# Kernel optimization log

Measured on AMD Instinct MI355X. Metric: run time of the kernel, lower is better.

The kernel has to match this reference:

```python
import jax, jax.numpy as jnp
import numpy as np

D = 256
H = 8
DH = D // H
TANH_CLIP = 10.0
NEG_INF = -1e9


def setup_inputs() -> dict:
    key = jax.random.key(0)
    ks = jax.random.split(key, 7)
    B, T, N = 32, 512, 512
    s = 1.0 / np.sqrt(D)
    return {
        "embeddings": jax.random.normal(ks[0], (B, N, D), dtype=jnp.float32),
        "current_nodes": jax.random.randint(ks[1], (B, T), 0, N, dtype=jnp.int64),
        "action_mask": jax.random.randint(ks[2], (B, T, N), 0, 2) > 0,
        "W_node": jax.random.normal(ks[3], (D, 3 * D), dtype=jnp.float32) * s,
        "W_fixed": jax.random.normal(ks[4], (D, D), dtype=jnp.float32) * s,
        "W_step": jax.random.normal(ks[5], (D, D), dtype=jnp.float32) * s,
        "W_out": jax.random.normal(ks[6], (D, D), dtype=jnp.float32) * s,
    }


def reference(embeddings, current_nodes, action_mask, W_node, W_fixed, W_step, W_out):
    """Batched equivalent of the autoregressive pointer-attention decode loop.

    embeddings: [B, N, D]; current_nodes: [B, T]; action_mask: [B, T, N] (True = feasible).
    Returns log_p: [B, T, N].
    """
    B, N, _ = embeddings.shape
    # ---- _precompute_cache ----
    proj = embeddings @ W_node                      # [B, N, 3D]
    glimpse_k, glimpse_v, logit_k = jnp.split(proj, 3, axis=-1)
    graph_context = jnp.mean(embeddings, axis=1) @ W_fixed   # [B, D]

    # ---- step context (gather current node embedding, project) ----
    step_emb = jnp.take_along_axis(embeddings, current_nodes[..., None], axis=1)  # [B, T, D]
    glimpse_q = step_emb @ W_step + graph_context[:, None, :]                      # [B, T, D]

    # ---- multi-head glimpse attention (one query per decode step) ----
    q = glimpse_q.reshape(B, -1, H, DH)
    k = glimpse_k.reshape(B, N, H, DH)
    v = glimpse_v.reshape(B, N, H, DH)
    scores = jnp.einsum("bthd,bnhd->bhtn", q, k) / np.sqrt(DH)
    scores = jnp.where(action_mask[:, None, :, :], scores, NEG_INF)
    attn = jax.nn.softmax(scores, axis=-1)
    heads = jnp.einsum("bhtn,bnhd->bthd", attn, v).reshape(B, -1, D)
    glimpse = heads @ W_out                                                        # [B, T, D]

    # ---- pointer logits: tanh clipping, mask, log-softmax ----
    logits = jnp.einsum("btd,bnd->btn", glimpse, logit_k) / np.sqrt(D)
    logits = TANH_CLIP * jnp.tanh(logits)
    logits = jnp.where(action_mask, logits, NEG_INF)
    return jax.nn.log_softmax(logits, axis=-1)
```

## Files before the change

kernel.cpp:

```cpp
#include <hip/hip_runtime.h>
#include <hip/hip_bf16.h>

constexpr int BB = 32;
constexpr int TT = 512;
constexpr int NN = 512;
constexpr int DD = 256;
constexpr int HH = 8;
constexpr int DH = 32;
#define NEG_INF (-1e9f)

#define QSCL 0.25505872f
#define LSCL 0.18033688f
#define MBF16 ((ushort)0xCE6E)

typedef __attribute__((ext_vector_type(8))) short bf16x8;
typedef __attribute__((ext_vector_type(4))) float f32x4;

__device__ inline float ex2(float x) { return __builtin_amdgcn_exp2f(x); }

__device__ inline ushort f2bf(float x) {
    union { float f; unsigned u; } c; c.f = x;
    unsigned u = c.u + 0x7fffu + ((c.u >> 16) & 1u);
    return (ushort)(u >> 16);
}
__device__ inline uint pk2t(float a, float b) {
    return __builtin_amdgcn_perm(__float_as_uint(b), __float_as_uint(a),
                                 0x07060302u);
}
__device__ inline ushort tr16(float x) { return (ushort)(__float_as_uint(x) >> 16); }
__device__ inline float bf2f(ushort u) {
    union { uint u; float f; } c; c.u = (uint)u << 16; return c.f;
}
__device__ inline void gload_lds16(const void* g, void* l) {
    __builtin_amdgcn_global_load_lds(
        (const __attribute__((address_space(1))) unsigned int*)g,
        (__attribute__((address_space(3))) unsigned int*)l, 16, 0, 0);
}

__global__ __launch_bounds__(256) void prep_all_k(
    const float* __restrict__ emb, ushort* __restrict__ embB,
    float* __restrict__ partial, const float* __restrict__ Wn,
    const float* __restrict__ Ws, const float* __restrict__ Wo,
    ushort* __restrict__ WnT, ushort* __restrict__ WsT,
    ushort* __restrict__ WoT, const int* __restrict__ mask,
    uint* __restrict__ mbt) {
    int j = blockIdx.x;
    int tid = threadIdx.x;
    if (j < 256) {
        int b = j >> 3, part = j & 7, d = tid;
        const float* eb = emb + ((size_t)b * NN + part * 64) * DD + d;
        ushort* ob = embB + ((size_t)b * NN + part * 64) * DD + d;
        float s = 0.f;
        #pragma unroll 4
        for (int i = 0; i < 64; i++) {
            float v = eb[(size_t)i * DD];
            s += v;
            ob[(size_t)i * DD] = f2bf(v);
        }
        partial[((size_t)b * 8 + part) * DD + d] = s;
    } else if (j < 576) {
        __shared__ float t[32][33];
        int g = j - 256;
        int gx = g % 40, gy = g / 40;
        const float* W;
        ushort* WT;
        int NC, xb;
        if (gx < 24)      { W = Wn; WT = WnT; NC = 768; xb = gx; }
        else if (gx < 32) { W = Ws; WT = WsT; NC = 256; xb = gx - 24; }
        else              { W = Wo; WT = WoT; NC = 256; xb = gx - 32; }
        int tx = tid & 31, ty = tid >> 5;
        int x = xb * 32 + tx;
        int y0 = gy * 32;
        #pragma unroll
        for (int i = 0; i < 4; i++)
            t[ty + i * 8][tx] = W[(size_t)(y0 + ty + i * 8) * NC + x];
        __syncthreads();
        #pragma unroll
        for (int i = 0; i < 4; i++)
            WT[(size_t)(xb * 32 + ty + i * 8) * 256 + y0 + tx] =
                f2bf(t[tx][ty + i * 8]);
    } else {
        int idx = (j - 576) * 256 + tid;
        int row = idx >> 4, w = idx & 15;
        const int* mr = mask + (size_t)row * NN + w;
        uint u = 0;
        #pragma unroll
        for (int c = 0; c < 32; c++) u |= (uint)(mr[c * 16] != 0) << c;
        mbt[idx] = u;
    }
}

template <int TASK>
__global__ __launch_bounds__(256) void gemm3_k(
    const ushort* __restrict__ A0, const ushort* __restrict__ WT0,
    const ushort* __restrict__ WT1, ushort* __restrict__ O0,
    ushort* __restrict__ O1, ushort* __restrict__ O2,
    ushort* __restrict__ O3, const float* __restrict__ partial,
    const float* __restrict__ Wf, const int* __restrict__ cur) {
    int j = blockIdx.x;
    bool k2 = (TASK == 0) && (j >= 1536);
    int bx, by;
    if (TASK == 0 && !k2) {
        int x = j & 7, t = j >> 3;
        bx = x * 16 + t / 12; by = t % 12;
    } else {
        int jj = k2 ? j - 1536 : j;
        int x = jj & 7, t = jj >> 3;
        bx = x * 16 + (t >> 2); by = t & 3;
    }
    int row0 = bx * 128, col0 = by * 64;
    int tid = threadIdx.x;
    int w = tid >> 6, l = tid & 63;
    int lo = l & 15, hi = l >> 4;

    __shared__ ushort As[2][128 * 64];
    __shared__ ushort Bs[2][64 * 64];
    __shared__ float ctxs[64];

    const ushort* WT = k2 ? WT1 : WT0;

    auto stage = [&](int buf, int kk) {
        #pragma unroll
        for (int i = 0; i < 4; i++) {
            int u = i * 256 + tid;
            int row = u >> 3, slot = u & 7;
            int arow = row0 + row;
            const ushort* ap;
            if (k2) {
                int b = arow >> 9;
                ap = A0 + ((size_t)(b * NN + cur[arow])) * DD;
            } else {
                ap = A0 + (size_t)arow * DD;
            }
            const void* gsrc = ap + kk * 64 + ((slot ^ (row & 7)) << 3);
            void* ldst = (char*)&As[buf][0] + i * 4096 + w * 1024;
            gload_lds16(gsrc, ldst);
        }
        #pragma unroll
        for (int i = 0; i < 2; i++) {
            int u = i * 256 + tid;
            int row = u >> 3, slot = u & 7;
            const void* gsrc =
                WT + (size_t)(col0 + row) * 256 + kk * 64 + ((slot ^ (row & 7)) << 3);
            void* ldst = (char*)&Bs[buf][0] + i * 4096 + w * 1024;
            gload_lds16(gsrc, ldst);
        }
    };

    const f32x4 zero = {0.f, 0.f, 0.f, 0.f};
    f32x4 acc[2][4] = {{zero, zero, zero, zero}, {zero, zero, zero, zero}};

    stage(0, 0);
    __syncthreads();
    #pragma unroll
    for (int kk = 0; kk < 4; kk++) {
        if (kk < 3) stage((kk + 1) & 1, kk + 1);
        int cb = kk & 1;
        #pragma unroll
        for (int ks = 0; ks < 2; ks++) {
            int sx = ((ks * 4 + hi) ^ (lo & 7)) << 4;
            bf16x8 af0 = *(const bf16x8*)((char*)&As[cb][0] + (w * 32 + lo) * 128 + sx);
            bf16x8 af1 = *(const bf16x8*)((char*)&As[cb][0] + (w * 32 + 16 + lo) * 128 + sx);
            #pragma unroll
            for (int c = 0; c < 4; c++) {
                bf16x8 bf = *(const bf16x8*)((char*)&Bs[cb][0] + (c * 16 + lo) * 128 + sx);
                acc[0][c] = __builtin_amdgcn_mfma_f32_16x16x32_bf16(af0, bf, acc[0][c], 0, 0, 0);
                acc[1][c] = __builtin_amdgcn_mfma_f32_16x16x32_bf16(af1, bf, acc[1][c], 0, 0, 0);
            }
        }
        __syncthreads();
    }

    int bbq = row0 >> 9;
    if (k2) {
        float* fs = (float*)&As[0][0];
        float mk = 0.f;
        #pragma unroll
        for (int p = 0; p < 8; p++)
            mk += partial[(size_t)bbq * 2048 + p * 256 + tid];
        fs[tid] = mk * (1.0f / 512.0f);
        __syncthreads();
        int cc = tid & 63, part = tid >> 6;
        float cs = 0.f;
        #pragma unroll 16
        for (int k = part * 64; k < part * 64 + 64; k++)
            cs += fs[k] * Wf[(size_t)k * 256 + col0 + cc];
        float* fs2 = fs + 256;
        fs2[part * 64 + cc] = cs;
        __syncthreads();
        if (tid < 64)
            ctxs[tid] = fs2[tid] + fs2[64 + tid] + fs2[128 + tid] + fs2[192 + tid];
        __syncthreads();
    }

    #pragma unroll
    for (int rg = 0; rg < 2; rg++) {
        int rw0 = row0 + w * 32 + rg * 16;
        int bb = rw0 >> 9;
        #pragma unroll
        for (int c = 0; c < 4; c++) {
            int col = col0 + c * 16 + lo;
            float v[4];
            #pragma unroll
            for (int r = 0; r < 4; r++) v[r] = acc[rg][c][r];
            if constexpr (TASK == 0) {
                if (k2) {
                    float bv = ctxs[col - col0];
                    #pragma unroll
                    for (int r = 0; r < 4; r++)
                        O3[(size_t)(rw0 + 4 * hi + r) * DD + col] =
                            f2bf((v[r] + bv) * QSCL);
                } else if (col < 256) {
                    int head = col >> 5, dh = col & 31;
                    #pragma unroll
                    for (int r = 0; r < 4; r++) {
                        int n = (rw0 + 4 * hi + r) & (NN - 1);
                        O0[(((size_t)(bb * HH + head) * NN + n) << 5) + dh] = f2bf(v[r]);
                    }
                } else if (col < 512) {
                    int cc2 = col - 256;
                    int bhv = bb * HH + (cc2 >> 5);
                    int dh = cc2 & 31;
                    int n0 = (rw0 + 4 * hi) & (NN - 1);
                    int m = n0 >> 2;
                    int p_ = m >> 3, s_ = (m >> 2) & 1, g_ = m & 3;
                    int n0p = (8 * p_ + 2 * g_ + s_) << 2;
                    ushort4 uv = {f2bf(v[0]), f2bf(v[1]), f2bf(v[2]), f2bf(v[3])};
                    *(ushort4*)(O1 + ((size_t)bhv * DH + dh) * NN + n0p) = uv;
                } else {
                    #pragma unroll
                    for (int r = 0; r < 4; r++)
                        O2[(size_t)(rw0 + 4 * hi + r) * 256 + (col - 512)] =
                            f2bf(v[r] * LSCL);
                }
            } else {
                #pragma unroll
                for (int r = 0; r < 4; r++)
                    O0[(size_t)(rw0 + 4 * hi + r) * DD + col] = f2bf(v[r]);
            }
        }
    }
}

__global__ __launch_bounds__(256, 4) void attn12_k(
    const ushort* __restrict__ gq, const ushort* __restrict__ gkT,
    const ushort* __restrict__ vTp, const uint* __restrict__ mbt,
    ushort* __restrict__ headsB) {
    int j = blockIdx.x;
    int bh = j & 255, quarter = j >> 8;
    int b = bh >> 3, h = bh & 7;
    int tid = threadIdx.x;
    int w = tid >> 6, l = tid & 63;
    int lo = l & 15, hi = l >> 4;

    __shared__ ushort Ks[8192];
    __shared__ ushort Vs[8192];
    __shared__ ushort OT[4][16][40];

    const f32x4 zero = {0.f, 0.f, 0.f, 0.f};
    const bf16x8 ones = {(short)0x3F80, (short)0x3F80, (short)0x3F80,
                         (short)0x3F80, (short)0x3F80, (short)0x3F80,
                         (short)0x3F80, (short)0x3F80};
    int q0 = quarter * 128;
    int kswz = (lo & 7) << 4;

    bf16x8 qf0 = *(const bf16x8*)(gq + ((size_t)(b * TT + q0 + w * 16 + lo)) * DD + h * DH + hi * 8);
    bf16x8 qf1 = *(const bf16x8*)(gq + ((size_t)(b * TT + q0 + 64 + w * 16 + lo)) * DD + h * DH + hi * 8);
    uint4 mq0 = *(const uint4*)(mbt + ((size_t)(b * TT + q0 + w * 16 + lo)) * 16 + 4 * hi);
    uint4 mq1 = *(const uint4*)(mbt + ((size_t)(b * TT + q0 + 64 + w * 16 + lo)) * 16 + 4 * hi);

    f32x4 o0[2] = {zero, zero};
    f32x4 o1[2] = {zero, zero};
    f32x4 osum[2] = {zero, zero};

    const char* kbase = (const char*)(gkT + (size_t)bh * (NN * DH));
    const char* vbase = (const char*)(vTp + (size_t)bh * (DH * NN));

    for (int ph = 0; ph < 2; ph++) {
        if (ph) __syncthreads();
        {
            const char* ksrc = kbase + ph * 16384;
            #pragma unroll
            for (int i = 0; i < 4; i++) {
                int x = (i * 256 + tid) * 16;
                int g = x ^ (((x >> 2) & 0x70) ^ ((x >> 4) & 0x10));
                gload_lds16(ksrc + g, (char*)Ks + i * 4096 + w * 1024);
            }
        }
        {
            const char* vsrc = vbase + ph * 512;
            #pragma unroll
            for (int i = 0; i < 4; i++) {
                int x = (i * 256 + tid) * 16;
                int g = ((x >> 9) << 10) + ((x & 511) ^ ((x >> 5) & 0x70));
                gload_lds16(vsrc + g, (char*)Vs + i * 4096 + w * 1024);
            }
        }
        __syncthreads();

        #pragma unroll
        for (int qc2 = 0; qc2 < 2; qc2++) {
            bf16x8 qf = qc2 ? qf1 : qf0;
            uint4 mq = qc2 ? mq1 : mq0;

            #pragma unroll 4
            for (int p = 0; p < 8; p++) {
                int nn = 32 * p + lo;
                bf16x8 kf0 = *(const bf16x8*)((char*)Ks + ((nn * 64 + hi * 16) ^ kswz));
                bf16x8 kf1 = *(const bf16x8*)((char*)Ks + (((nn + 16) * 64 + hi * 16) ^ kswz));
                __builtin_amdgcn_s_setprio(1);
                f32x4 s0 = __builtin_amdgcn_mfma_f32_16x16x32_bf16(kf0, qf, zero, 0, 0, 0);
                f32x4 s1 = __builtin_amdgcn_mfma_f32_16x16x32_bf16(kf1, qf, zero, 0, 0, 0);
                __builtin_amdgcn_s_setprio(0);
                union { bf16x8 v; uint u[4]; } pf;
                {
                    int c = ph * 16 + 2 * p;
                    float e0 = ((mq.x >> c) & 1u) ? ex2(s0[0]) : 0.f;
                    float e1 = ((mq.y >> c) & 1u) ? ex2(s0[1]) : 0.f;
                    float e2 = ((mq.z >> c) & 1u) ? ex2(s0[2]) : 0.f;
                    float e3 = ((mq.w >> c) & 1u) ? ex2(s0[3]) : 0.f;
                    pf.u[0] = pk2t(e0, e1);
                    pf.u[1] = pk2t(e2, e3);
                }
                {
                    int c = ph * 16 + 2 * p + 1;
                    float e0 = ((mq.x >> c) & 1u) ? ex2(s1[0]) : 0.f;
                    float e1 = ((mq.y >> c) & 1u) ? ex2(s1[1]) : 0.f;
                    float e2 = ((mq.z >> c) & 1u) ? ex2(s1[2]) : 0.f;
                    float e3 = ((mq.w >> c) & 1u) ? ex2(s1[3]) : 0.f;
                    pf.u[2] = pk2t(e0, e1);
                    pf.u[3] = pk2t(e2, e3);
                }
                int vo = (32 * p + 8 * hi) * 2;
                bf16x8 va0 = *(const bf16x8*)((char*)Vs + ((lo * 512 + vo) ^ kswz));
                bf16x8 va1 = *(const bf16x8*)((char*)Vs + (((lo + 16) * 512 + vo) ^ kswz));
                __builtin_amdgcn_s_setprio(1);
                o0[qc2] = __builtin_amdgcn_mfma_f32_16x16x32_bf16(va0, pf.v, o0[qc2], 0, 0, 0);
                o1[qc2] = __builtin_amdgcn_mfma_f32_16x16x32_bf16(va1, pf.v, o1[qc2], 0, 0, 0);
                osum[qc2] = __builtin_amdgcn_mfma_f32_16x16x32_bf16(ones, pf.v, osum[qc2], 0, 0, 0);
                __builtin_amdgcn_s_setprio(0);
            }
        }
    }

    #pragma unroll
    for (int qc2 = 0; qc2 < 2; qc2++) {
        int t0 = q0 + qc2 * 64 + w * 16;
        float inv = 1.0f / fmaxf(osum[qc2][0], 1e-30f);
        #pragma unroll
        for (int r = 0; r < 4; r++) {
            OT[w][lo][4 * hi + r] = tr16(o0[qc2][r] * inv);
            OT[w][lo][16 + 4 * hi + r] = tr16(o1[qc2][r] * inv);
        }
        bf16x8 ov = *(const bf16x8*)(&OT[w][lo][hi * 8]);
        *(bf16x8*)(headsB + ((size_t)(b * TT + t0 + lo)) * DD + h * DH + hi * 8) = ov;
    }
}

__global__ __launch_bounds__(256) void logits_mm_k(
    const ushort* __restrict__ glimpse, const ushort* __restrict__ lkb,
    const uint* __restrict__ mbt, ushort* __restrict__ logitsB,
    float* __restrict__ psum) {
    int j = blockIdx.x;
    int x = j & 7, t = j >> 3;
    int b = x * 4 + (t >> 5);
    int rem = t & 31;
    int bx = rem >> 3, by = rem & 7;
    int row0 = bx * 128, col0 = by * 64;
    int tid = threadIdx.x;
    int w = tid >> 6, l = tid & 63;
    int lo = l & 15, hi = l >> 4;

    __shared__ ushort As[2][128 * 64];
    __shared__ ushort Bs[2][64 * 64];

    const ushort* Abase = glimpse + (size_t)b * TT * DD;
    const ushort* Bbase = lkb + (size_t)b * NN * DD;

    auto stage = [&](int buf, int kk) {
        #pragma unroll
        for (int i = 0; i < 4; i++) {
            int u = i * 256 + tid;
            int row = u >> 3, slot = u & 7;
            const void* gsrc =
                Abase + (size_t)(row0 + row) * DD + kk * 64 + ((slot ^ (row & 7)) << 3);
            void* ldst = (char*)&As[buf][0] + i * 4096 + w * 1024;
            gload_lds16(gsrc, ldst);
        }
        #pragma unroll
        for (int i = 0; i < 2; i++) {
            int u = i * 256 + tid;
            int row = u >> 3, slot = u & 7;
            const void* gsrc =
                Bbase + (size_t)(col0 + row) * DD + kk * 64 + ((slot ^ (row & 7)) << 3);
            void* ldst = (char*)&Bs[buf][0] + i * 4096 + w * 1024;
            gload_lds16(gsrc, ldst);
        }
    };

    const f32x4 zero = {0.f, 0.f, 0.f, 0.f};
    f32x4 acc[2][4] = {{zero, zero, zero, zero}, {zero, zero, zero, zero}};

    stage(0, 0);
    __syncthreads();
    #pragma unroll
    for (int kk = 0; kk < 4; kk++) {
        if (kk < 3) stage((kk + 1) & 1, kk + 1);
        int cb = kk & 1;
        #pragma unroll
        for (int ks = 0; ks < 2; ks++) {
            int sx = ((ks * 4 + hi) ^ (lo & 7)) << 4;
            bf16x8 af0 = *(const bf16x8*)((char*)&As[cb][0] + (w * 32 + lo) * 128 + sx);
            bf16x8 af1 = *(const bf16x8*)((char*)&As[cb][0] + (w * 32 + 16 + lo) * 128 + sx);
            #pragma unroll
            for (int c = 0; c < 4; c++) {
                bf16x8 bf = *(const bf16x8*)((char*)&Bs[cb][0] + (c * 16 + lo) * 128 + sx);
                acc[0][c] = __builtin_amdgcn_mfma_f32_16x16x32_bf16(af0, bf, acc[0][c], 0, 0, 0);
                acc[1][c] = __builtin_amdgcn_mfma_f32_16x16x32_bf16(af1, bf, acc[1][c], 0, 0, 0);
            }
        }
        __syncthreads();
    }

    #pragma unroll
    for (int rg = 0; rg < 2; rg++) {
        int rw = row0 + w * 32 + rg * 16;
        uint mw[4];
        #pragma unroll
        for (int r = 0; r < 4; r++)
            mw[r] = mbt[((size_t)(b * TT + rw + 4 * hi + r)) * 16 + lo];
        float rsum[4] = {0.f, 0.f, 0.f, 0.f};
        #pragma unroll
        for (int c = 0; c < 4; c++) {
            int col = col0 + c * 16 + lo;
            int cg = by * 4 + c;
            #pragma unroll
            for (int r = 0; r < 4; r++) {
                float y = fminf(fmaxf(acc[rg][c][r], -57.f), 57.f);
                float t2 = 10.f - 20.f / (ex2(y) + 1.f);
                uint bit = (mw[r] >> cg) & 1u;
                logitsB[((size_t)(b * TT + rw + 4 * hi + r)) * NN + col] =
                    bit ? tr16(t2) : MBF16;
                rsum[r] += bit ? __expf(t2 - 10.f) : 0.f;
            }
        }
        #pragma unroll
        for (int r = 0; r < 4; r++) {
            #pragma unroll
            for (int o = 1; o < 16; o <<= 1) rsum[r] += __shfl_xor(rsum[r], o);
        }
        if (lo == 0) {
            #pragma unroll
            for (int r = 0; r < 4; r++)
                psum[((size_t)(b * TT + rw + 4 * hi + r)) * 8 + by] = rsum[r];
        }
    }
}

__global__ __launch_bounds__(256) void logits_fin_k(
    const ushort* __restrict__ logitsB, const float* __restrict__ psum,
    float* __restrict__ out) {
    int r0 = blockIdx.x * 8;
    int tid = threadIdx.x;
    __shared__ float lsev[8];
    if (tid < 8) {
        const float* pp = psum + (size_t)(r0 + tid) * 8;
        float s = 0.f;
        #pragma unroll
        for (int p = 0; p < 8; p++) s += pp[p];
        lsev[tid] = 10.f + __logf(fmaxf(s, 1e-37f));
    }
    __syncthreads();
    int row = tid >> 5, n0 = (tid & 31) * 16;
    float lse = lsev[row];
    const ushort* lb = logitsB + (size_t)(r0 + row) * NN + n0;
    bf16x8 v0 = *(const bf16x8*)(lb);
    bf16x8 v1 = *(const bf16x8*)(lb + 8);
    float ov[16];
    #pragma unroll
    for (int jj = 0; jj < 16; jj++) {
        float lv = bf2f((ushort)(jj < 8 ? v0[jj] : v1[jj - 8]));
        ov[jj] = lv - lse;
    }
    float* ob = out + (size_t)(r0 + row) * NN + n0;
    #pragma unroll
    for (int q = 0; q < 4; q++)
        *(float4*)(ob + q * 4) = *(float4*)(&ov[q * 4]);
}

extern "C" void kernel_launch(void* const* d_in, const int* in_sizes, int n_in,
                              void* d_out, int out_size, void* d_ws,
                              size_t ws_size, hipStream_t stream) {
    const float* emb = (const float*)d_in[0];
    const int* cur   = (const int*)d_in[1];
    const int* mask  = (const int*)d_in[2];
    const float* Wn  = (const float*)d_in[3];
    const float* Wf  = (const float*)d_in[4];
    const float* Ws  = (const float*)d_in[5];
    const float* Wo  = (const float*)d_in[6];
    float* out = (float*)d_out;

    const size_t SLABE = (size_t)BB * NN * DD;
    ushort* embB     = (ushort*)d_ws;
    ushort* gkT      = embB + SLABE;
    ushort* vTp      = gkT + SLABE;
    ushort* lkb      = vTp + SLABE;
    ushort* gq       = lkb + SLABE;
    ushort* headsB   = gq + SLABE;
    ushort* glimpseB = headsB + SLABE;
    ushort* WnT      = glimpseB + SLABE;
    ushort* WsT      = WnT + 768 * 256;
    ushort* WoT      = WsT + 256 * 256;
    uint*   mbt      = (uint*)(WoT + 256 * 256);
    float*  partial  = (float*)(mbt + (size_t)BB * TT * 16);
    ushort* logitsB  = embB;
    float*  psum     = (float*)(embB + (size_t)BB * TT * NN);

    prep_all_k<<<1600, 256, 0, stream>>>(emb, embB, partial, Wn, Ws, Wo,
                                         WnT, WsT, WoT, mask, mbt);
    gemm3_k<0><<<2048, 256, 0, stream>>>(embB, WnT, WsT, gkT, vTp, lkb, gq,
                                         partial, Wf, cur);
    attn12_k<<<1024, 256, 0, stream>>>(gq, gkT, vTp, mbt, headsB);
    gemm3_k<1><<<512, 256, 0, stream>>>(headsB, WoT, nullptr, glimpseB,
                                        nullptr, nullptr, nullptr, nullptr,
                                        nullptr, nullptr);
    logits_mm_k<<<1024, 256, 0, stream>>>(glimpseB, lkb, mbt, logitsB, psum);
    logits_fin_k<<<BB * TT / 8, 256, 0, stream>>>(logitsB, psum, out);
}
```

Measured before the change: 101.5 us.

## Fuse pointer-logit GEMM and log-softmax finalize into one full-row kernel

Replaces the two-kernel logits path (tiled GEMM writing bf16 logits plus partial sums, then a finalize pass) with one kernel. Each block now owns 32 full rows across all 512 columns, keeps the tanh-clipped logits packed in registers, reduces the row sum in LDS and writes the final fp32 log-probabilities directly. This removes the bf16 logits round trip through global memory and one launch. In exchange the grid is halved to 512 blocks, each block does more serial work, and register and LDS pressure rise, which may lower occupancy.

```diff
diff --git a/kernel.cpp b/kernel.cpp
--- a/kernel.cpp
+++ b/kernel.cpp
@@ -11,7 +11,6 @@
 
 #define QSCL 0.25505872f
 #define LSCL 0.18033688f
-#define MBF16 ((ushort)0xCE6E)
 
 typedef __attribute__((ext_vector_type(8))) short bf16x8;
 typedef __attribute__((ext_vector_type(4))) float f32x4;
@@ -28,8 +27,11 @@
                                  0x07060302u);
 }
 __device__ inline ushort tr16(float x) { return (ushort)(__float_as_uint(x) >> 16); }
-__device__ inline float bf2f(ushort u) {
-    union { uint u; float f; } c; c.u = (uint)u << 16; return c.f;
+__device__ inline float ulo(uint u) {
+    union { uint u; float f; } c; c.u = u << 16; return c.f;
+}
+__device__ inline float uhi(uint u) {
+    union { uint u; float f; } c; c.u = u & 0xffff0000u; return c.f;
 }
 __device__ inline void gload_lds16(const void* g, void* l) {
     __builtin_amdgcn_global_load_lds(
@@ -357,135 +359,131 @@
     }
 }
 
-__global__ __launch_bounds__(256) void logits_mm_k(
+__global__ __launch_bounds__(256) void logits7_k(
     const ushort* __restrict__ glimpse, const ushort* __restrict__ lkb,
-    const uint* __restrict__ mbt, ushort* __restrict__ logitsB,
-    float* __restrict__ psum) {
+    const uint* __restrict__ mbt, float* __restrict__ out) {
     int j = blockIdx.x;
     int x = j & 7, t = j >> 3;
-    int b = x * 4 + (t >> 5);
-    int rem = t & 31;
-    int bx = rem >> 3, by = rem & 7;
-    int row0 = bx * 128, col0 = by * 64;
+    int b = x * 4 + (t >> 4);
+    int row0 = (t & 15) * 32;
     int tid = threadIdx.x;
     int w = tid >> 6, l = tid & 63;
     int lo = l & 15, hi = l >> 4;
 
-    __shared__ ushort As[2][128 * 64];
-    __shared__ ushort Bs[2][64 * 64];
-
-    const ushort* Abase = glimpse + (size_t)b * TT * DD;
+    __shared__ ushort As[32 * 256];
+    __shared__ ushort Bs[2][64 * 256];
+    __shared__ float reds[4][2][16];
+
+    const ushort* Abase = glimpse + ((size_t)b * TT + row0) * DD;
     const ushort* Bbase = lkb + (size_t)b * NN * DD;
-
-    auto stage = [&](int buf, int kk) {
-        #pragma unroll
-        for (int i = 0; i < 4; i++) {
-            int u = i * 256 + tid;
-            int row = u >> 3, slot = u & 7;
-            const void* gsrc =
-                Abase + (size_t)(row0 + row) * DD + kk * 64 + ((slot ^ (row & 7)) << 3);
-            void* ldst = (char*)&As[buf][0] + i * 4096 + w * 1024;
-            gload_lds16(gsrc, ldst);
-        }
-        #pragma unroll
-        for (int i = 0; i < 2; i++) {
-            int u = i * 256 + tid;
-            int row = u >> 3, slot = u & 7;
-            const void* gsrc =
-                Bbase + (size_t)(col0 + row) * DD + kk * 64 + ((slot ^ (row & 7)) << 3);
-            void* ldst = (char*)&Bs[buf][0] + i * 4096 + w * 1024;
-            gload_lds16(gsrc, ldst);
+    int kswz = (lo & 7) << 4;
+
+    #pragma unroll
+    for (int i = 0; i < 4; i++) {
+        int xx = (i * 256 + tid) * 16;
+        int g = xx ^ ((xx >> 5) & 0x70);
+        gload_lds16((const char*)Abase + g, (char*)As + i * 4096 + w * 1024);
+    }
+    auto stageB = [&](int buf, int p) {
+        const char* src = (const char*)(Bbase + (size_t)p * 64 * DD);
+        #pragma unroll
+        for (int i = 0; i < 8; i++) {
+            int xx = (i * 256 + tid) * 16;
+            int g = xx ^ ((xx >> 5) & 0x70);
+            gload_lds16(src + g, (char*)&Bs[buf][0] + i * 4096 + w * 1024);
         }
     };
+    stageB(0, 0);
+    __syncthreads();
+
+    bf16x8 af0[8], af1[8];
+    #pragma unroll
+    for (int ks = 0; ks < 8; ks++) {
+        int sx = ((ks * 4 + hi) << 4) ^ kswz;
+        af0[ks] = *(const bf16x8*)((char*)As + lo * 512 + sx);
+        af1[ks] = *(const bf16x8*)((char*)As + (16 + lo) * 512 + sx);
+    }
+    uint mw0[4], mw1[4];
+    #pragma unroll
+    for (int r = 0; r < 4; r++) {
+        mw0[r] = mbt[((size_t)(b * TT + row0 + 4 * hi + r)) * 16 + lo];
+        mw1[r] = mbt[((size_t)(b * TT + row0 + 16 + 4 * hi + r)) * 16 + lo];
+    }
 
     const f32x4 zero = {0.f, 0.f, 0.f, 0.f};
-    f32x4 acc[2][4] = {{zero, zero, zero, zero}, {zero, zero, zero, zero}};
-
-    stage(0, 0);
+    float sum0[4] = {0.f, 0.f, 0.f, 0.f}, sum1[4] = {0.f, 0.f, 0.f, 0.f};
+    uint tuA[8], tuB[8], tuC[8], tuD[8];
+
+    #pragma unroll
+    for (int p = 0; p < 8; p++) {
+        if (p < 7) stageB((p + 1) & 1, p + 1);
+        int cb = p & 1;
+        f32x4 a0 = zero, a1 = zero;
+        #pragma unroll
+        for (int ks = 0; ks < 8; ks++) {
+            int sx = ((ks * 4 + hi) << 4) ^ kswz;
+            bf16x8 bf = *(const bf16x8*)((char*)&Bs[cb][0] + (w * 16 + lo) * 512 + sx);
+            a0 = __builtin_amdgcn_mfma_f32_16x16x32_bf16(af0[ks], bf, a0, 0, 0, 0);
+            a1 = __builtin_amdgcn_mfma_f32_16x16x32_bf16(af1[ks], bf, a1, 0, 0, 0);
+        }
+        int c = p * 4 + w;
+        float t0v[4], t1v[4];
+        #pragma unroll
+        for (int r = 0; r < 4; r++) {
+            float y0 = fminf(fmaxf(a0[r], -57.f), 57.f);
+            float y1 = fminf(fmaxf(a1[r], -57.f), 57.f);
+            t0v[r] = 10.f - 20.f / (ex2(y0) + 1.f);
+            t1v[r] = 10.f - 20.f / (ex2(y1) + 1.f);
+            sum0[r] += ((mw0[r] >> c) & 1u) ? __expf(t0v[r] - 10.f) : 0.f;
+            sum1[r] += ((mw1[r] >> c) & 1u) ? __expf(t1v[r] - 10.f) : 0.f;
+        }
+        tuA[p] = pk2t(t0v[0], t0v[1]);
+        tuB[p] = pk2t(t0v[2], t0v[3]);
+        tuC[p] = pk2t(t1v[0], t1v[1]);
+        tuD[p] = pk2t(t1v[2], t1v[3]);
+        __syncthreads();
+    }
+
+    #pragma unroll
+    for (int r = 0; r < 4; r++) {
+        #pragma unroll
+        for (int o = 1; o < 16; o <<= 1) {
+            sum0[r] += __shfl_xor(sum0[r], o);
+            sum1[r] += __shfl_xor(sum1[r], o);
+        }
+    }
+    if (lo == 0) {
+        #pragma unroll
+        for (int r = 0; r < 4; r++) {
+            reds[w][0][4 * hi + r] = sum0[r];
+            reds[w][1][4 * hi + r] = sum1[r];
+        }
+    }
     __syncthreads();
-    #pragma unroll
-    for (int kk = 0; kk < 4; kk++) {
-        if (kk < 3) stage((kk + 1) & 1, kk + 1);
-        int cb = kk & 1;
-        #pragma unroll
-        for (int ks = 0; ks < 2; ks++) {
-            int sx = ((ks * 4 + hi) ^ (lo & 7)) << 4;
-            bf16x8 af0 = *(const bf16x8*)((char*)&As[cb][0] + (w * 32 + lo) * 128 + sx);
-            bf16x8 af1 = *(const bf16x8*)((char*)&As[cb][0] + (w * 32 + 16 + lo) * 128 + sx);
-            #pragma unroll
-            for (int c = 0; c < 4; c++) {
-                bf16x8 bf = *(const bf16x8*)((char*)&Bs[cb][0] + (c * 16 + lo) * 128 + sx);
-                acc[0][c] = __builtin_amdgcn_mfma_f32_16x16x32_bf16(af0, bf, acc[0][c], 0, 0, 0);
-                acc[1][c] = __builtin_amdgcn_mfma_f32_16x16x32_bf16(af1, bf, acc[1][c], 0, 0, 0);
-            }
-        }
-        __syncthreads();
-    }
-
-    #pragma unroll
-    for (int rg = 0; rg < 2; rg++) {
-        int rw = row0 + w * 32 + rg * 16;
-        uint mw[4];
-        #pragma unroll
-        for (int r = 0; r < 4; r++)
-            mw[r] = mbt[((size_t)(b * TT + rw + 4 * hi + r)) * 16 + lo];
-        float rsum[4] = {0.f, 0.f, 0.f, 0.f};
-        #pragma unroll
-        for (int c = 0; c < 4; c++) {
-            int col = col0 + c * 16 + lo;
-            int cg = by * 4 + c;
-            #pragma unroll
-            for (int r = 0; r < 4; r++) {
-                float y = fminf(fmaxf(acc[rg][c][r], -57.f), 57.f);
-                float t2 = 10.f - 20.f / (ex2(y) + 1.f);
-                uint bit = (mw[r] >> cg) & 1u;
-                logitsB[((size_t)(b * TT + rw + 4 * hi + r)) * NN + col] =
-                    bit ? tr16(t2) : MBF16;
-                rsum[r] += bit ? __expf(t2 - 10.f) : 0.f;
-            }
-        }
+    float lse0[4], lse1[4];
+    #pragma unroll
+    for (int r = 0; r < 4; r++) {
+        int row = 4 * hi + r;
+        lse0[r] = 10.f + __logf(fmaxf(reds[0][0][row] + reds[1][0][row] +
+                                      reds[2][0][row] + reds[3][0][row], 1e-37f));
+        lse1[r] = 10.f + __logf(fmaxf(reds[0][1][row] + reds[1][1][row] +
+                                      reds[2][1][row] + reds[3][1][row], 1e-37f));
+    }
+
+    #pragma unroll
+    for (int p = 0; p < 8; p++) {
+        int c = p * 4 + w;
+        int col = p * 64 + w * 16 + lo;
+        float v0[4] = {ulo(tuA[p]), uhi(tuA[p]), ulo(tuB[p]), uhi(tuB[p])};
+        float v1[4] = {ulo(tuC[p]), uhi(tuC[p]), ulo(tuD[p]), uhi(tuD[p])};
         #pragma unroll
         for (int r = 0; r < 4; r++) {
-            #pragma unroll
-            for (int o = 1; o < 16; o <<= 1) rsum[r] += __shfl_xor(rsum[r], o);
-        }
-        if (lo == 0) {
-            #pragma unroll
-            for (int r = 0; r < 4; r++)
-                psum[((size_t)(b * TT + rw + 4 * hi + r)) * 8 + by] = rsum[r];
-        }
-    }
-}
-
-__global__ __launch_bounds__(256) void logits_fin_k(
-    const ushort* __restrict__ logitsB, const float* __restrict__ psum,
-    float* __restrict__ out) {
-    int r0 = blockIdx.x * 8;
-    int tid = threadIdx.x;
-    __shared__ float lsev[8];
-    if (tid < 8) {
-        const float* pp = psum + (size_t)(r0 + tid) * 8;
-        float s = 0.f;
-        #pragma unroll
-        for (int p = 0; p < 8; p++) s += pp[p];
-        lsev[tid] = 10.f + __logf(fmaxf(s, 1e-37f));
-    }
-    __syncthreads();
-    int row = tid >> 5, n0 = (tid & 31) * 16;
-    float lse = lsev[row];
-    const ushort* lb = logitsB + (size_t)(r0 + row) * NN + n0;
-    bf16x8 v0 = *(const bf16x8*)(lb);
-    bf16x8 v1 = *(const bf16x8*)(lb + 8);
-    float ov[16];
-    #pragma unroll
-    for (int jj = 0; jj < 16; jj++) {
-        float lv = bf2f((ushort)(jj < 8 ? v0[jj] : v1[jj - 8]));
-        ov[jj] = lv - lse;
-    }
-    float* ob = out + (size_t)(r0 + row) * NN + n0;
-    #pragma unroll
-    for (int q = 0; q < 4; q++)
-        *(float4*)(ob + q * 4) = *(float4*)(&ov[q * 4]);
+            float ov0 = ((mw0[r] >> c) & 1u) ? v0[r] - lse0[r] : NEG_INF - lse0[r];
+            float ov1 = ((mw1[r] >> c) & 1u) ? v1[r] - lse1[r] : NEG_INF - lse1[r];
+            out[((size_t)(b * TT + row0 + 4 * hi + r)) * NN + col] = ov0;
+            out[((size_t)(b * TT + row0 + 16 + 4 * hi + r)) * NN + col] = ov1;
+        }
+    }
 }
 
 extern "C" void kernel_launch(void* const* d_in, const int* in_sizes, int n_in,
@@ -513,8 +511,6 @@
     ushort* WoT      = WsT + 256 * 256;
     uint*   mbt      = (uint*)(WoT + 256 * 256);
     float*  partial  = (float*)(mbt + (size_t)BB * TT * 16);
-    ushort* logitsB  = embB;
-    float*  psum     = (float*)(embB + (size_t)BB * TT * NN);
 
     prep_all_k<<<1600, 256, 0, stream>>>(emb, embB, partial, Wn, Ws, Wo,
                                          WnT, WsT, WoT, mask, mbt);
@@ -524,6 +520,5 @@
     gemm3_k<1><<<512, 256, 0, stream>>>(headsB, WoT, nullptr, glimpseB,
                                         nullptr, nullptr, nullptr, nullptr,
                                         nullptr, nullptr);
-    logits_mm_k<<<1024, 256, 0, stream>>>(glimpseB, lkb, mbt, logitsB, psum);
-    logits_fin_k<<<BB * TT / 8, 256, 0, stream>>>(logitsB, psum, out);
-}
+    logits7_k<<<512, 256, 0, stream>>>(glimpseB, lkb, mbt, out);
+}
```

Result: faster. 95.71 us (-5.7%).
